# Optimization experiments

Measured on AMD Instinct MI355X. Metric: run time of the kernel, lower is better.

Reference implementation:

```python
import jax, jax.numpy as jnp
import numpy as np

TEMP = 0.5
WEIGHT = (0.4, 0.3, 0.3)


def _l2norm(x):
    n = jnp.linalg.norm(x, axis=-1, keepdims=True)
    return x / jnp.maximum(n, 1e-12)


def _forward(st_i, st_j, car_i, car_j, pl_i, pl_j, gt_labels,
             cen_st, cen_car, cen_pl, conc):
    w = jnp.asarray(WEIGHT, dtype=st_i.dtype)[:, None, None]  # [3,1,1]
    feats = [jnp.concatenate([_l2norm(a), _l2norm(b)], axis=0)
             for a, b in ((st_i, st_j), (car_i, car_j), (pl_i, pl_j))]  # each [N,D]
    sims = jnp.stack([f @ f.T for f in feats])  # [3,N,N]
    wmask = jnp.where(sims == 0, jnp.zeros_like(w), w)
    wsim = (sims * wmask).sum(0) / (wmask.sum(0) + 1e-12)  # [N,N]
    e = jnp.exp(wsim / TEMP)
    N = e.shape[0]
    B = N // 2
    idx = jnp.arange(N)
    pos = e[idx, (idx + B) % N]  # positive_mask gather: one positive per row
    # negative_mask excludes diagonal and the positive -> row sum minus both
    neg_sum = e.sum(-1) - e[idx, idx] - pos
    loss = (-jnp.log(pos / (pos + neg_sum))).mean()

    # prototype branch: gt_labels covers all C clusters, unique set == arange(C)
    labels = gt_labels[:, 0]  # [N]
    C = cen_st.shape[0]
    k = jnp.arange(C - 1)
    neg_ids = k[None, :] + (k[None, :] >= labels[:, None]).astype(k.dtype)  # sorted ids != label
    proto_ids = jnp.concatenate([labels[:, None], neg_ids], axis=1)  # [N,C], col 0 = positive
    logits = jnp.stack([
        jnp.take_along_axis(f @ c.T, proto_ids, axis=1)
        for f, c in zip(feats, (cen_st, cen_car, cen_pl))])  # [3,N,C]
    temp_proto = conc[:, proto_ids]  # [3,N,C]
    logits = logits / (temp_proto + 1e-12)
    w2 = jnp.where((temp_proto == 0) | (logits == 0), jnp.zeros_like(w), w)
    logits_w = (logits * w2).sum(0) / (w2.sum(0) + 1e-12)  # [N,C]
    # CrossEntropyLoss(mean) with target class 0 for every row
    loss_proto = (-jax.nn.log_softmax(logits_w, axis=-1)[:, 0]).mean()
    return loss + loss_proto


def setup_inputs() -> dict:
    key = jax.random.key(0)
    ks = jax.random.split(key, 12)
    B, D, C = 2048, 128, 512
    N = 2 * B
    inp = {}
    names = ['st_feat_i', 'st_feat_j', 'car_feat_i', 'car_feat_j',
             'plate_feat_i', 'plate_feat_j']
    for i, nm in enumerate(names):
        inp[nm] = jax.random.normal(ks[i], (B, D), dtype=jnp.float32)
    # labels covering all C clusters so torch.unique(gt_labels) == arange(C)
    labels = jnp.tile(jnp.arange(C, dtype=jnp.int32), N // C)
    labels = jax.random.permutation(ks[6], labels)
    inp['gt_labels'] = labels[:, None]
    inp['st_centroids'] = jax.random.normal(ks[7], (C, D), dtype=jnp.float32)
    inp['car_centroids'] = jax.random.normal(ks[8], (C, D), dtype=jnp.float32)
    inp['plate_centroids'] = jax.random.normal(ks[9], (C, D), dtype=jnp.float32)
    inp['concentration'] = jax.random.uniform(ks[10], (3, C), dtype=jnp.float32,
                                              minval=0.1, maxval=1.0)
    return inp


def reference(st_feat_i, st_feat_j, car_feat_i, car_feat_j,
              plate_feat_i, plate_feat_j, gt_labels,
              st_centroids, car_centroids, plate_centroids, concentration):
    return _forward(st_feat_i, st_feat_j, car_feat_i, car_feat_j,
                    plate_feat_i, plate_feat_j, gt_labels,
                    st_centroids, car_centroids, plate_centroids, concentration)
```

## Files before the change

kernel.cpp:

```cpp
#include <hip/hip_runtime.h>
#include <hip/hip_bf16.h>
#include <math.h>

#define BB 2048
#define NN 4096
#define DD 128
#define CC 512
#define NSIM 528

typedef __attribute__((ext_vector_type(8))) short bf16x8;
typedef __attribute__((ext_vector_type(4))) float f32x4;

__global__ __launch_bounds__(256) void k_normprep(
    const float* __restrict__ si, const float* __restrict__ sj,
    const float* __restrict__ ci, const float* __restrict__ cj,
    const float* __restrict__ pi, const float* __restrict__ pj,
    const float* __restrict__ cst, const float* __restrict__ cca,
    const float* __restrict__ cpl, const float* __restrict__ conc,
    __hip_bfloat16* __restrict__ fbf, __hip_bfloat16* __restrict__ cbf) {
  const int m   = blockIdx.y;
  const int tid = threadIdx.x;
  const int w   = tid >> 6;
  const int t   = tid & 63;
  const float sqw = (m == 0) ? 0.632455532033676f : 0.547722557505166f;
  if (blockIdx.x < NN / 4) {
    const int row = blockIdx.x * 4 + w;
    const float* src;
    if (m == 0)      src = (row < BB) ? si : sj;
    else if (m == 1) src = (row < BB) ? ci : cj;
    else             src = (row < BB) ? pi : pj;
    const int r = (row < BB) ? row : row - BB;
    float2 v = ((const float2*)(src + (size_t)r * DD))[t];
    float ss = v.x * v.x + v.y * v.y;
    #pragma unroll
    for (int k = 32; k >= 1; k >>= 1) ss += __shfl_xor(ss, k);
    const float inv = sqw / fmaxf(sqrtf(ss), 1e-12f);
    __hip_bfloat16* db = fbf + (size_t)m * NN * DD + (size_t)row * DD;
    db[2 * t]     = __float2bfloat16(v.x * inv);
    db[2 * t + 1] = __float2bfloat16(v.y * inv);
  } else {
    const int crow = (blockIdx.x - NN / 4) * 4 + w;
    const float* src = (m == 0) ? cst : (m == 1) ? cca : cpl;
    const float sc = sqw / (conc[m * CC + crow] + 1e-12f);
    float2 v = ((const float2*)(src + (size_t)crow * DD))[t];
    __hip_bfloat16* db = cbf + (size_t)m * CC * DD + (size_t)crow * DD;
    db[2 * t]     = __float2bfloat16(v.x * sc);
    db[2 * t + 1] = __float2bfloat16(v.y * sc);
  }
}

__global__ __launch_bounds__(256, 3) void k_main(const __hip_bfloat16* __restrict__ fbf,
                                                 const __hip_bfloat16* __restrict__ cbf,
                                                 const int* __restrict__ labels,
                                                 float* __restrict__ rowsum,
                                                 float* __restrict__ pos_e,
                                                 float* __restrict__ diag_e,
                                                 float* __restrict__ pmax_g,
                                                 float* __restrict__ psum_g,
                                                 float* __restrict__ zl_g) {
  __shared__ bf16x8 As[1024];
  __shared__ bf16x8 Bs[1024];

  const int tid  = threadIdx.x;
  const int lane = tid & 63;
  const int wid  = tid >> 6;
  const int l15  = lane & 15;
  const int kg   = lane >> 4;

  if (blockIdx.x < NSIM) {
    int tB = blockIdx.x;
    int by = 0;
    while (tB >= 32 - by) { tB -= 32 - by; ++by; }
    const int bx = by + tB;
    const bool diag = (by == bx);
    const int rowBase = by * 128;
    const int colBase = bx * 128;

    const int wr = wid >> 1, wc = wid & 1;
    const int srow = tid >> 3;
    const int kc   = tid & 7;
    const int sc   = kc ^ (srow & 7);

    f32x4 acc[4][4] = {};
    bf16x8 ra[4], rb[4];

    {
      const __hip_bfloat16* F = fbf;
      #pragma unroll
      for (int q = 0; q < 4; ++q) {
        ra[q] = *(const bf16x8*)(F + (size_t)(rowBase + q * 32 + srow) * DD + kc * 8);
        if (!diag)
          rb[q] = *(const bf16x8*)(F + (size_t)(colBase + q * 32 + srow) * DD + kc * 8);
      }
    }

    for (int t = 0; t < 6; ++t) {
      #pragma unroll
      for (int q = 0; q < 4; ++q) {
        As[(q * 32 + srow) * 8 + sc] = ra[q];
        if (!diag) Bs[(q * 32 + srow) * 8 + sc] = rb[q];
      }
      __syncthreads();

      if (t < 5) {
        const __hip_bfloat16* F = fbf + (size_t)((t + 1) >> 1) * NN * DD + ((t + 1) & 1) * 64;
        #pragma unroll
        for (int q = 0; q < 4; ++q) {
          ra[q] = *(const bf16x8*)(F + (size_t)(rowBase + q * 32 + srow) * DD + kc * 8);
          if (!diag)
            rb[q] = *(const bf16x8*)(F + (size_t)(colBase + q * 32 + srow) * DD + kc * 8);
        }
      }

      const bf16x8* Bsrc = diag ? As : Bs;
      #pragma unroll
      for (int ks2 = 0; ks2 < 2; ++ks2) {
        bf16x8 a[4], b[4];
        const int ch = (ks2 * 4 + kg) ^ (l15 & 7);
        #pragma unroll
        for (int ti = 0; ti < 4; ++ti)
          a[ti] = As[(wr * 64 + ti * 16 + l15) * 8 + ch];
        #pragma unroll
        for (int tj = 0; tj < 4; ++tj)
          b[tj] = Bsrc[(wc * 64 + tj * 16 + l15) * 8 + ch];
        #pragma unroll
        for (int ti = 0; ti < 4; ++ti)
          #pragma unroll
          for (int tj = 0; tj < 4; ++tj)
            acc[ti][tj] = __builtin_amdgcn_mfma_f32_16x16x32_bf16(a[ti], b[tj], acc[ti][tj], 0, 0, 0);
      }
      __syncthreads();
    }

    float csum[4] = {0.f, 0.f, 0.f, 0.f};
    #pragma unroll
    for (int ti = 0; ti < 4; ++ti) {
      #pragma unroll
      for (int j = 0; j < 4; ++j) {
        const int i = rowBase + wr * 64 + ti * 16 + kg * 4 + j;
        float rsum = 0.f;
        #pragma unroll
        for (int tj = 0; tj < 4; ++tj) {
          const int jcol = colBase + wc * 64 + tj * 16 + l15;
          const float e = expf(2.0f * acc[ti][tj][j]);
          rsum += e;
          csum[tj] += e;
          if (diag) {
            if (jcol == i) diag_e[i] = e;
          } else if (jcol == ((i + BB) & (NN - 1))) {
            pos_e[i] = e;
            pos_e[jcol] = e;
          }
        }
        #pragma unroll
        for (int msk = 8; msk >= 1; msk >>= 1) rsum += __shfl_xor(rsum, msk);
        if (l15 == 0) atomicAdd(&rowsum[i], rsum);
      }
    }
    if (!diag) {
      #pragma unroll
      for (int tj = 0; tj < 4; ++tj) {
        float v = csum[tj];
        v += __shfl_xor(v, 16);
        v += __shfl_xor(v, 32);
        if (lane < 16) atomicAdd(&rowsum[colBase + wc * 64 + tj * 16 + l15], v);
      }
    }
  } else {
    float* wmaxs = (float*)As;
    float* wsums = wmaxs + 64;
    int*   slab  = (int*)(wsums + 64);

    const int bidp = blockIdx.x - NSIM;
    const int half = bidp & 1;
    const int row0 = (bidp >> 1) * 16;
    const int cbase = half * 256 + wid * 64;

    if (tid < 16) slab[tid] = labels[row0 + tid];
    __syncthreads();

    f32x4 acc[4] = {};
    #pragma unroll
    for (int ks = 0; ks < 12; ++ks) {
      const int koff = (ks & 3) * 32 + kg * 8;
      const __hip_bfloat16* F  = fbf + (size_t)(ks >> 2) * NN * DD + koff;
      const __hip_bfloat16* Cm = cbf + (size_t)(ks >> 2) * CC * DD + koff;
      const bf16x8 af = *(const bf16x8*)(F + (size_t)(row0 + l15) * DD);
      bf16x8 bf_[4];
      #pragma unroll
      for (int tj = 0; tj < 4; ++tj)
        bf_[tj] = *(const bf16x8*)(Cm + (size_t)(cbase + tj * 16 + l15) * DD);
      #pragma unroll
      for (int tj = 0; tj < 4; ++tj)
        acc[tj] = __builtin_amdgcn_mfma_f32_16x16x32_bf16(af, bf_[tj], acc[tj], 0, 0, 0);
    }

    #pragma unroll
    for (int j = 0; j < 4; ++j) {
      const int r = kg * 4 + j;
      #pragma unroll
      for (int tj = 0; tj < 4; ++tj) {
        const int c = cbase + tj * 16 + l15;
        if (c == slab[r]) zl_g[row0 + r] = acc[tj][j];
      }
    }

    #pragma unroll
    for (int j = 0; j < 4; ++j) {
      float mx = acc[0][j];
      #pragma unroll
      for (int tj = 1; tj < 4; ++tj) mx = fmaxf(mx, acc[tj][j]);
      #pragma unroll
      for (int msk = 8; msk >= 1; msk >>= 1) mx = fmaxf(mx, __shfl_xor(mx, msk));
      if (l15 == 0) wmaxs[wid * 16 + kg * 4 + j] = mx;
    }
    __syncthreads();

    #pragma unroll
    for (int j = 0; j < 4; ++j) {
      const int r = kg * 4 + j;
      const float bmx = fmaxf(fmaxf(wmaxs[0 * 16 + r], wmaxs[1 * 16 + r]),
                              fmaxf(wmaxs[2 * 16 + r], wmaxs[3 * 16 + r]));
      float se = 0.f;
      #pragma unroll
      for (int tj = 0; tj < 4; ++tj) se += expf(acc[tj][j] - bmx);
      #pragma unroll
      for (int msk = 8; msk >= 1; msk >>= 1) se += __shfl_xor(se, msk);
      if (l15 == 0) wsums[wid * 16 + r] = se;
    }
    __syncthreads();

    if (tid < 16) {
      const int r = tid;
      const float bmx = fmaxf(fmaxf(wmaxs[0 * 16 + r], wmaxs[1 * 16 + r]),
                              fmaxf(wmaxs[2 * 16 + r], wmaxs[3 * 16 + r]));
      const float s = wsums[0 * 16 + r] + wsums[1 * 16 + r] +
                      wsums[2 * 16 + r] + wsums[3 * 16 + r];
      pmax_g[(size_t)half * NN + row0 + r] = bmx;
      psum_g[(size_t)half * NN + row0 + r] = s;
    }
  }
}

__global__ void k_final(const float* __restrict__ rowsum, const float* __restrict__ pos_e,
                        const float* __restrict__ diag_e, const float* __restrict__ pmax_g,
                        const float* __restrict__ psum_g, const float* __restrict__ zl_g,
                        float* __restrict__ out) {
  __shared__ float redA[4], redB[4];
  const int tid = threadIdx.x;
  float sa = 0.f, sb = 0.f;
  for (int i = tid; i < NN; i += 256) {
    sa += logf(rowsum[i] - diag_e[i]) - logf(pos_e[i]);
    const float m0 = pmax_g[i], m1 = pmax_g[NN + i];
    const float M = fmaxf(m0, m1);
    const float s = psum_g[i] * expf(m0 - M) + psum_g[NN + i] * expf(m1 - M);
    sb += M + logf(s) - zl_g[i];
  }
  const int lane = tid & 63, wv = tid >> 6;
  #pragma unroll
  for (int k = 32; k >= 1; k >>= 1) { sa += __shfl_xor(sa, k); sb += __shfl_xor(sb, k); }
  if (lane == 0) { redA[wv] = sa; redB[wv] = sb; }
  __syncthreads();
  if (tid == 0) {
    const float la = redA[0] + redA[1] + redA[2] + redA[3];
    const float lb = redB[0] + redB[1] + redB[2] + redB[3];
    out[0] = la / (float)NN + lb / (float)NN;
  }
}

extern "C" void kernel_launch(void* const* d_in, const int* in_sizes, int n_in,
                              void* d_out, int out_size, void* d_ws, size_t ws_size,
                              hipStream_t stream) {
  (void)in_sizes; (void)n_in; (void)out_size; (void)ws_size;
  const float* si  = (const float*)d_in[0];
  const float* sj  = (const float*)d_in[1];
  const float* ci  = (const float*)d_in[2];
  const float* cj  = (const float*)d_in[3];
  const float* pi  = (const float*)d_in[4];
  const float* pj  = (const float*)d_in[5];
  const int*   lab = (const int*)d_in[6];
  const float* cst = (const float*)d_in[7];
  const float* cca = (const float*)d_in[8];
  const float* cpl = (const float*)d_in[9];
  const float* cnc = (const float*)d_in[10];

  float* ws     = (float*)d_ws;
  float* rowsum = ws;
  float* pos_e  = rowsum + NN;
  float* diag_e = pos_e + NN;
  float* pmax_g = diag_e + NN;
  float* psum_g = pmax_g + 2 * NN;
  float* zl_g   = psum_g + 2 * NN;
  __hip_bfloat16* fbf = (__hip_bfloat16*)(zl_g + NN);
  __hip_bfloat16* cbf = fbf + (size_t)3 * NN * DD;

  hipMemsetAsync(rowsum, 0, NN * sizeof(float), stream);

  k_normprep<<<dim3(NN / 4 + CC / 4, 3), 256, 0, stream>>>(si, sj, ci, cj, pi, pj,
                                                           cst, cca, cpl, cnc, fbf, cbf);
  k_main<<<NSIM + 2 * (NN / 16), 256, 0, stream>>>(fbf, cbf, lab, rowsum, pos_e, diag_e,
                                                   pmax_g, psum_g, zl_g);
  k_final<<<1, 256, 0, stream>>>(rowsum, pos_e, diag_e, pmax_g, psum_g, zl_g, (float*)d_out);
}
```

Before: 126.9 us.

## Enlarge prototype tiles to 64 rows, fold rowsum zeroing into prep kernel

Each prototype-branch block in the main kernel now computes 64 feature rows instead of 16, reusing the loaded centroid fragments across four row tiles. This cuts the prototype block count from 512 to 128 and reduces redundant centroid loads. The separate memset of rowsum is removed, and zeroing moves into the normalisation kernel, which now runs 512-thread blocks over 8 rows each. The larger accumulator array (64 floats per thread) raises register pressure and may reduce occupancy or cause spills under the existing launch bounds.

New measurement: 118.9 us (median of 2 runs). -6.3%, faster.

```diff
diff --git a/kernel.cpp b/kernel.cpp
--- a/kernel.cpp
+++ b/kernel.cpp
@@ -7,24 +7,32 @@
 #define DD 128
 #define CC 512
 #define NSIM 528
+#define NPROTO 128
 
 typedef __attribute__((ext_vector_type(8))) short bf16x8;
 typedef __attribute__((ext_vector_type(4))) float f32x4;
 
-__global__ __launch_bounds__(256) void k_normprep(
+__global__ __launch_bounds__(512) void k_normprep(
     const float* __restrict__ si, const float* __restrict__ sj,
     const float* __restrict__ ci, const float* __restrict__ cj,
     const float* __restrict__ pi, const float* __restrict__ pj,
     const float* __restrict__ cst, const float* __restrict__ cca,
     const float* __restrict__ cpl, const float* __restrict__ conc,
-    __hip_bfloat16* __restrict__ fbf, __hip_bfloat16* __restrict__ cbf) {
+    __hip_bfloat16* __restrict__ fbf, __hip_bfloat16* __restrict__ cbf,
+    float* __restrict__ rowsum) {
   const int m   = blockIdx.y;
   const int tid = threadIdx.x;
   const int w   = tid >> 6;
   const int t   = tid & 63;
   const float sqw = (m == 0) ? 0.632455532033676f : 0.547722557505166f;
-  if (blockIdx.x < NN / 4) {
-    const int row = blockIdx.x * 4 + w;
+
+  if (m == 2 && blockIdx.x < 2) {
+    const int i = (blockIdx.x * 512 + tid) * 4;
+    *(float4*)(rowsum + i) = make_float4(0.f, 0.f, 0.f, 0.f);
+  }
+
+  if (blockIdx.x < NN / 8) {
+    const int row = blockIdx.x * 8 + w;
     const float* src;
     if (m == 0)      src = (row < BB) ? si : sj;
     else if (m == 1) src = (row < BB) ? ci : cj;
@@ -39,7 +47,7 @@
     db[2 * t]     = __float2bfloat16(v.x * inv);
     db[2 * t + 1] = __float2bfloat16(v.y * inv);
   } else {
-    const int crow = (blockIdx.x - NN / 4) * 4 + w;
+    const int crow = (blockIdx.x - NN / 8) * 8 + w;
     const float* src = (m == 0) ? cst : (m == 1) ? cca : cpl;
     const float sc = sqw / (conc[m * CC + crow] + 1e-12f);
     float2 v = ((const float2*)(src + (size_t)crow * DD))[t];
@@ -168,74 +176,88 @@
     }
   } else {
     float* wmaxs = (float*)As;
-    float* wsums = wmaxs + 64;
-    int*   slab  = (int*)(wsums + 64);
+    float* wsums = wmaxs + 256;
+    int*   slab  = (int*)(wsums + 256);
 
     const int bidp = blockIdx.x - NSIM;
     const int half = bidp & 1;
-    const int row0 = (bidp >> 1) * 16;
+    const int row0 = (bidp >> 1) * 64;
     const int cbase = half * 256 + wid * 64;
 
-    if (tid < 16) slab[tid] = labels[row0 + tid];
+    if (tid < 64) slab[tid] = labels[row0 + tid];
     __syncthreads();
 
-    f32x4 acc[4] = {};
+    f32x4 acc[4][4] = {};
     #pragma unroll
     for (int ks = 0; ks < 12; ++ks) {
       const int koff = (ks & 3) * 32 + kg * 8;
       const __hip_bfloat16* F  = fbf + (size_t)(ks >> 2) * NN * DD + koff;
       const __hip_bfloat16* Cm = cbf + (size_t)(ks >> 2) * CC * DD + koff;
-      const bf16x8 af = *(const bf16x8*)(F + (size_t)(row0 + l15) * DD);
-      bf16x8 bf_[4];
+      bf16x8 af[4], bfr[4];
+      #pragma unroll
+      for (int ti = 0; ti < 4; ++ti)
+        af[ti] = *(const bf16x8*)(F + (size_t)(row0 + ti * 16 + l15) * DD);
       #pragma unroll
       for (int tj = 0; tj < 4; ++tj)
-        bf_[tj] = *(const bf16x8*)(Cm + (size_t)(cbase + tj * 16 + l15) * DD);
-      #pragma unroll
-      for (int tj = 0; tj < 4; ++tj)
-        acc[tj] = __builtin_amdgcn_mfma_f32_16x16x32_bf16(af, bf_[tj], acc[tj], 0, 0, 0);
-    }
-
-    #pragma unroll
-    for (int j = 0; j < 4; ++j) {
-      const int r = kg * 4 + j;
-      #pragma unroll
-      for (int tj = 0; tj < 4; ++tj) {
-        const int c = cbase + tj * 16 + l15;
-        if (c == slab[r]) zl_g[row0 + r] = acc[tj][j];
-      }
-    }
-
-    #pragma unroll
-    for (int j = 0; j < 4; ++j) {
-      float mx = acc[0][j];
-      #pragma unroll
-      for (int tj = 1; tj < 4; ++tj) mx = fmaxf(mx, acc[tj][j]);
-      #pragma unroll
-      for (int msk = 8; msk >= 1; msk >>= 1) mx = fmaxf(mx, __shfl_xor(mx, msk));
-      if (l15 == 0) wmaxs[wid * 16 + kg * 4 + j] = mx;
+        bfr[tj] = *(const bf16x8*)(Cm + (size_t)(cbase + tj * 16 + l15) * DD);
+      #pragma unroll
+      for (int ti = 0; ti < 4; ++ti)
+        #pragma unroll
+        for (int tj = 0; tj < 4; ++tj)
+          acc[ti][tj] = __builtin_amdgcn_mfma_f32_16x16x32_bf16(af[ti], bfr[tj], acc[ti][tj], 0, 0, 0);
+    }
+
+    #pragma unroll
+    for (int ti = 0; ti < 4; ++ti) {
+      #pragma unroll
+      for (int j = 0; j < 4; ++j) {
+        const int r = ti * 16 + kg * 4 + j;
+        #pragma unroll
+        for (int tj = 0; tj < 4; ++tj) {
+          const int c = cbase + tj * 16 + l15;
+          if (c == slab[r]) zl_g[row0 + r] = acc[ti][tj][j];
+        }
+      }
+    }
+
+    #pragma unroll
+    for (int ti = 0; ti < 4; ++ti) {
+      #pragma unroll
+      for (int j = 0; j < 4; ++j) {
+        const int r = ti * 16 + kg * 4 + j;
+        float mx = acc[ti][0][j];
+        #pragma unroll
+        for (int tj = 1; tj < 4; ++tj) mx = fmaxf(mx, acc[ti][tj][j]);
+        #pragma unroll
+        for (int msk = 8; msk >= 1; msk >>= 1) mx = fmaxf(mx, __shfl_xor(mx, msk));
+        if (l15 == 0) wmaxs[wid * 64 + r] = mx;
+      }
     }
     __syncthreads();
 
     #pragma unroll
-    for (int j = 0; j < 4; ++j) {
-      const int r = kg * 4 + j;
-      const float bmx = fmaxf(fmaxf(wmaxs[0 * 16 + r], wmaxs[1 * 16 + r]),
-                              fmaxf(wmaxs[2 * 16 + r], wmaxs[3 * 16 + r]));
-      float se = 0.f;
-      #pragma unroll
-      for (int tj = 0; tj < 4; ++tj) se += expf(acc[tj][j] - bmx);
-      #pragma unroll
-      for (int msk = 8; msk >= 1; msk >>= 1) se += __shfl_xor(se, msk);
-      if (l15 == 0) wsums[wid * 16 + r] = se;
+    for (int ti = 0; ti < 4; ++ti) {
+      #pragma unroll
+      for (int j = 0; j < 4; ++j) {
+        const int r = ti * 16 + kg * 4 + j;
+        const float bmx = fmaxf(fmaxf(wmaxs[0 * 64 + r], wmaxs[1 * 64 + r]),
+                                fmaxf(wmaxs[2 * 64 + r], wmaxs[3 * 64 + r]));
+        float se = 0.f;
+        #pragma unroll
+        for (int tj = 0; tj < 4; ++tj) se += expf(acc[ti][tj][j] - bmx);
+        #pragma unroll
+        for (int msk = 8; msk >= 1; msk >>= 1) se += __shfl_xor(se, msk);
+        if (l15 == 0) wsums[wid * 64 + r] = se;
+      }
     }
     __syncthreads();
 
-    if (tid < 16) {
+    if (tid < 64) {
       const int r = tid;
-      const float bmx = fmaxf(fmaxf(wmaxs[0 * 16 + r], wmaxs[1 * 16 + r]),
-                              fmaxf(wmaxs[2 * 16 + r], wmaxs[3 * 16 + r]));
-      const float s = wsums[0 * 16 + r] + wsums[1 * 16 + r] +
-                      wsums[2 * 16 + r] + wsums[3 * 16 + r];
+      const float bmx = fmaxf(fmaxf(wmaxs[0 * 64 + r], wmaxs[1 * 64 + r]),
+                              fmaxf(wmaxs[2 * 64 + r], wmaxs[3 * 64 + r]));
+      const float s = wsums[0 * 64 + r] + wsums[1 * 64 + r] +
+                      wsums[2 * 64 + r] + wsums[3 * 64 + r];
       pmax_g[(size_t)half * NN + row0 + r] = bmx;
       psum_g[(size_t)half * NN + row0 + r] = s;
     }
@@ -294,11 +316,9 @@
   __hip_bfloat16* fbf = (__hip_bfloat16*)(zl_g + NN);
   __hip_bfloat16* cbf = fbf + (size_t)3 * NN * DD;
 
-  hipMemsetAsync(rowsum, 0, NN * sizeof(float), stream);
-
-  k_normprep<<<dim3(NN / 4 + CC / 4, 3), 256, 0, stream>>>(si, sj, ci, cj, pi, pj,
-                                                           cst, cca, cpl, cnc, fbf, cbf);
-  k_main<<<NSIM + 2 * (NN / 16), 256, 0, stream>>>(fbf, cbf, lab, rowsum, pos_e, diag_e,
-                                                   pmax_g, psum_g, zl_g);
+  k_normprep<<<dim3(NN / 8 + CC / 8, 3), 512, 0, stream>>>(si, sj, ci, cj, pi, pj,
+                                                           cst, cca, cpl, cnc, fbf, cbf, rowsum);
+  k_main<<<NSIM + NPROTO, 256, 0, stream>>>(fbf, cbf, lab, rowsum, pos_e, diag_e,
+                                            pmax_g, psum_g, zl_g);
   k_final<<<1, 256, 0, stream>>>(rowsum, pos_e, diag_e, pmax_g, psum_g, zl_g, (float*)d_out);
 }
```
